# Performance work log

Hardware: AMD Instinct MI355X
Metric: run time of the kernel (lower is better)

The kernel has to match this reference:

```python
import jax, jax.numpy as jnp
import numpy as np

SR = 48000.0


def _lin_interp(x, n):
    # Matches torch F.interpolate(mode='linear', align_corners=False) on last axis.
    T = x.shape[-1]
    pos = (jnp.arange(n, dtype=jnp.float32) + 0.5) * (T / n) - 0.5
    pos = jnp.clip(pos, 0.0, T - 1)
    i0 = jnp.floor(pos).astype(jnp.int32)
    i1 = jnp.minimum(i0 + 1, T - 1)
    w = (pos - i0.astype(jnp.float32)).astype(x.dtype)
    return jnp.take(x, i0, axis=-1) * (1.0 - w) + jnp.take(x, i1, axis=-1) * w


def setup_inputs() -> dict:
    key = jax.random.key(0)
    k1, k2, k3 = jax.random.split(key, 3)
    B, T, N = 16, 250, 100
    harm_amps = jax.random.uniform(k1, (B, T, N), dtype=jnp.float32)
    # realistic fundamental frequencies: 80..480 Hz
    f0_hz = 80.0 + 400.0 * jax.random.uniform(k2, (B, T), dtype=jnp.float32)
    # small inharmonicity coefficients (piano-like): ~0..1e-4
    inh = 1e-4 * jax.random.uniform(k3, (B,), dtype=jnp.float32)
    return {"harm_amps": harm_amps, "f0_hz": f0_hz, "inh": inh, "n_samples": 48000}


def reference(harm_amps, f0_hz, inh, n_samples):
    B, T, N = harm_amps.shape
    # upsample amplitudes (B,N,n_samples) and f0 (B,n_samples)
    a = _lin_interp(jnp.transpose(harm_amps, (0, 2, 1)), n_samples)
    f0_up = _lin_interp(f0_hz, n_samples)
    k = jnp.arange(1, N + 1, dtype=jnp.float32)  # harmonic numbers 1..N
    stretch = jnp.sqrt(1.0 + inh[:, None] * k ** 2)  # (B,N)
    inst_freq = f0_up[:, None, :] * (k[None, :] * stretch)[:, :, None]  # (B,N,n)
    nyq_mask = (inst_freq < SR * 0.45).astype(a.dtype)
    phase = jnp.cumsum(2.0 * jnp.pi * inst_freq / SR, axis=-1)
    signal = jnp.sum(a * nyq_mask * jnp.sin(phase), axis=1, keepdims=True)  # (B,1,n)
    return signal / N
```

## Files before the change

kernel.cpp:

```cpp
#include <hip/hip_runtime.h>
#include <cmath>

#pragma clang fp contract(off)

#define SRF   48000.0f
#define NYQF  21600.0f
constexpr float  TWO_PI_F  = 6.283185307179586476925286766559f;
constexpr double INV_2PI_D = 0.15915494309189533576888376337251;
constexpr float  RC1 = (float)INV_2PI_D;
constexpr float  RC2 = (float)(INV_2PI_D - (double)RC1);
constexpr double INV_SR_D = 1.0 / 48000.0;
constexpr float  DD1 = (float)INV_SR_D;
constexpr float  DD2 = (float)(INV_SR_D - (double)DD1);

__device__ __forceinline__ float hsin_rev(float r) {
#if __has_builtin(__builtin_amdgcn_sinf)
    return __builtin_amdgcn_sinf(r);
#else
    return __sinf(r * TWO_PI_F);
#endif
}

__device__ __forceinline__ float div48000(float t) {
    float h = t * DD1;
    float r = __builtin_fmaf(t, DD1, -h);
    float s = __builtin_fmaf(t, DD2, r);
    return h + s;
}

__device__ __forceinline__ float sin_phase(float ph) {
    float h  = ph * RC1;
    float r  = __builtin_fmaf(ph, RC1, -h);
    float s  = __builtin_fmaf(ph, RC2, r);
    float nn = __builtin_rintf(h);
    float fr = (h - nn) + s;
    return hsin_rev(fr);
}

template <int IDX>
__device__ __forceinline__ float grp4_bcast(float v, int lb) {
#if __has_builtin(__builtin_amdgcn_ds_swizzle)
    constexpr int imm = (IDX << 5) | 0x1C;
    return __int_as_float(__builtin_amdgcn_ds_swizzle(__float_as_int(v), imm));
#else
    return __shfl(v, lb + IDX);
#endif
}

__device__ __forceinline__ float grp8_bcast0(float v, int lane) {
#if __has_builtin(__builtin_amdgcn_ds_swizzle)
    return __int_as_float(__builtin_amdgcn_ds_swizzle(__float_as_int(v), 0x0018));
#else
    return __shfl(v, lane & ~7);
#endif
}

__device__ __forceinline__ float pair_swap(float v) {
#if __has_builtin(__builtin_amdgcn_ds_swizzle)
    return __int_as_float(__builtin_amdgcn_ds_swizzle(__float_as_int(v), 0x041F));
#else
    return __shfl_xor(v, 1);
#endif
}

__device__ __forceinline__ float kcval(int k, float ib) {
    float kf = (float)(k + 1);
    float k2 = kf * kf;
    float m  = ib * k2;
    float s1 = 1.0f + m;
    float st = (float)sqrt((double)s1);
    return kf * st;
}

__global__ void __launch_bounds__(256) k_f0up(const float* __restrict__ f0,
        float* __restrict__ f0up, float* __restrict__ out,
        int T, int n, float pf) {
    int j = blockIdx.x * 256 + threadIdx.x;
    int b = blockIdx.y;
    if (j >= n) return;
    float pos = ((float)j + 0.5f);
    pos = pos * pf;
    pos = pos - 0.5f;
    pos = fmaxf(pos, 0.0f);
    pos = fminf(pos, (float)(T - 1));
    int   i0 = (int)pos;
    int   i1 = min(i0 + 1, T - 1);
    float w  = pos - (float)i0;
    float omw = 1.0f - w;
    const float* fb = f0 + b * T;
    f0up[(size_t)b * n + j] = fb[i0] * omw + fb[i1] * w;
    out[(size_t)b * n + j]  = 0.0f;
}

__global__ void __launch_bounds__(256) k_scan4(const float* __restrict__ f0up,
        const float* __restrict__ inh, float* __restrict__ scanS,
        int N, int n) {
    __shared__ float lv[3008];
    const int k   = blockIdx.x;
    const int b   = blockIdx.y;
    const int tid = threadIdx.x;
    const float kc = kcval(k, inh[b]);
    const float4* f4 = (const float4*)(f0up + (size_t)b * n);
    const int len4 = n >> 4;
    const int len5 = n >> 5;

    auto l2of = [&](float4 v) -> float {
        float a0 = div48000(TWO_PI_F * (kc * v.x));
        float a1 = div48000(TWO_PI_F * (kc * v.y));
        float a2 = div48000(TWO_PI_F * (kc * v.z));
        float a3 = div48000(TWO_PI_F * (kc * v.w));
        return (a0 + a1) + (a2 + a3);
    };
    auto l4of = [&](int j) -> float {
        float s01 = l2of(f4[4*j])     + l2of(f4[4*j + 1]);
        float s23 = l2of(f4[4*j + 2]) + l2of(f4[4*j + 3]);
        return s01 + s23;
    };
    for (int i = tid; i < len4; i += 256) {
        float v  = l4of(i);
        float vp = pair_swap(v);
        if ((i & 1) == 0) lv[i >> 1] = v + vp;
    }
    __syncthreads();

    int offp = 0, lenp = len5, P = 5;
    for (int l = 6; ; ++l) {
        int lenc = lenp >> 1;
        int offc = offp + lenp;
        for (int i = tid; i < lenc; i += 256)
            lv[offc + i] = lv[offp + 2*i] + lv[offp + 2*i + 1];
        __syncthreads();
        P = l;
        if (lenc == 1) break;
        offp = offc; lenp = lenc;
    }
    for (int l = P - 1; l >= 5; --l) {
        int lenl = n >> l;
        int offl = 0;
        for (int m = 5; m < l; ++m) offl += (n >> m);
        float*       arr = lv + offl;
        const float* hi  = lv + offl + lenl;
        int lenh = n >> (l + 1);
        for (int i = tid; i < lenh; i += 256) {
            float v = hi[i];
            int e = 2*i + 2;
            if (e < lenl) arr[e] = v + arr[e];
            arr[2*i + 1] = v;
        }
        __syncthreads();
    }
    float* sp = scanS + (size_t)(b * N + k) * (len5 + 1);
    if (tid == 0) sp[0] = 0.0f;
    for (int i = tid; i < len5; i += 256) sp[1 + i] = lv[i];
}

__global__ void __launch_bounds__(256) k_synth4(
        const float* __restrict__ harm, const float* __restrict__ f0up,
        const float* __restrict__ inh,  const float* __restrict__ scanS,
        float* __restrict__ out, int B, int T, int N, int n, float pf, int kpg) {
    const int tid  = threadIdx.x;
    const int b    = blockIdx.y;
    const int k0   = blockIdx.z * kpg;
    const int g    = blockIdx.x * 256 + tid;
    const int q    = g >> 2;
    const int c    = g & 3;
    const int NG   = n >> 4;
    const int NG5P = (n >> 5) + 1;
    const int kend = min(k0 + kpg, N);
    const int kact = kend - k0;
    const bool valid = q < NG;
    const bool oddq  = (q & 1) != 0;
    const int  si    = (q >> 1) + (q & 1);

    __shared__ float2 amps[8 * 32];
    __shared__ float  kcs[32];
    __shared__ float  xp[4][256];

    const float ib    = inh[b];
    const float tmaxf = (float)(T - 1);
    for (int i = tid; i < kact; i += 256) kcs[i] = kcval(k0 + i, ib);

    const int j0blk = blockIdx.x * 1024;
    int i0min;
    {
        float p = ((float)j0blk + 0.5f);
        p = p * pf; p = p - 0.5f;
        p = fmaxf(p, 0.0f); p = fminf(p, tmaxf);
        i0min = (int)p;
    }
    for (int idx = tid; idx < 8 * kact; idx += 256) {
        int r = idx / kact, kk = idx - r * kact;
        int r0 = min(i0min + r, T - 1);
        int r1 = min(i0min + r + 1, T - 1);
        float a0 = harm[((size_t)b * T + r0) * N + (k0 + kk)];
        float a1 = harm[((size_t)b * T + r1) * N + (k0 + kk)];
        amps[idx] = make_float2(a0, a1 - a0);
    }
    __syncthreads();

    float u0=0.f,u1=0.f,u2=0.f,u3=0.f;
    float w0=0.f,w1=0.f,w2=0.f,w3=0.f;
    int   a0o=0,a1o=0,a2o=0,a3o=0;
    float acc0=0.f, acc1=0.f, acc2=0.f, acc3=0.f;
    float um = __builtin_inff();
    if (valid) {
        const float4 v = *(const float4*)(f0up + (size_t)b * n + (size_t)q * 16 + c * 4);
        u0=v.x; u1=v.y; u2=v.z; u3=v.w;
        um = fminf(fminf(u0,u1), fminf(u2,u3));
        const int jb = q * 16 + c * 4;
        #pragma unroll
        for (int i = 0; i < 4; ++i) {
            float p = ((float)(jb + i) + 0.5f);
            p = p * pf; p = p - 0.5f;
            p = fmaxf(p, 0.0f); p = fminf(p, tmaxf);
            int i0 = (int)p;
            float wv = p - (float)i0;
            int aoo  = (i0 - i0min) * kact;
            if (i==0){w0=wv;a0o=aoo;}
            else if (i==1){w1=wv;a1o=aoo;}
            else if (i==2){w2=wv;a2o=aoo;}
            else {w3=wv;a3o=aoo;}
        }
    }
    #pragma unroll
    for (int off = 32; off > 0; off >>= 1)
        um = fminf(um, __shfl_xor(um, off));
    const float umin = um;
    const int lane = tid & 63;
    const int lb   = lane & ~3;

    if (valid) {
        const float* s4k = scanS + (size_t)(b * N + k0) * NG5P;
        float svc = s4k[si];

        for (int k = k0; k < kend; ++k) {
            const int   kk = k - k0;
            const float kc = kcs[kk];
            if (kc * umin >= NYQF) break;
            const float Sv = svc;
            if (k + 1 < kend) {
                const float* nx = s4k + NG5P;
                svc = nx[si];
                s4k = nx;
            }

            float x0 = div48000(TWO_PI_F * (kc * u0));
            float x1 = div48000(TWO_PI_F * (kc * u1));
            float x2 = div48000(TWO_PI_F * (kc * u2));
            float x3 = div48000(TWO_PI_F * (kc * u3));
            float L1p = x0 + x1, L1q = x2 + x3;
            float L2  = L1p + L1q;

            float s0 = grp4_bcast<0>(L2, lb);
            float s1 = grp4_bcast<1>(L2, lb);
            float s2 = grp4_bcast<2>(L2, lb);
            float s3 = grp4_bcast<3>(L2, lb);
            float t01 = s0 + s1;
            float s23 = s2 + s3;
            float L4v = t01 + s23;
            float G1e = Sv + L4v;
            float Gx  = grp8_bcast0(G1e, lane);
            float G0  = oddq ? Gx : Sv;
            float G1  = oddq ? Sv : G1e;

            float b1v = G0 + s0;
            float b2v = G0 + t01;
            float b3v = b2v + s2;
            float base = (c == 0) ? G0  : (c == 1) ? b1v : (c == 2) ? b2v : b3v;
            float bn   = (c == 0) ? b1v : (c == 1) ? b2v : (c == 2) ? b3v : G1;

            float ph0 = base + x0;
            float ph1 = base + L1p;
            float ph2 = ph1 + x2;
            float ph3 = bn;

            {   float t1 = kc * u0;
                if (t1 < NYQF) { float sv = sin_phase(ph0);
                    float2 a = amps[a0o + kk];
                    acc0 = __builtin_fmaf(__builtin_fmaf(w0, a.y, a.x), sv, acc0); } }
            {   float t1 = kc * u1;
                if (t1 < NYQF) { float sv = sin_phase(ph1);
                    float2 a = amps[a1o + kk];
                    acc1 = __builtin_fmaf(__builtin_fmaf(w1, a.y, a.x), sv, acc1); } }
            {   float t1 = kc * u2;
                if (t1 < NYQF) { float sv = sin_phase(ph2);
                    float2 a = amps[a2o + kk];
                    acc2 = __builtin_fmaf(__builtin_fmaf(w2, a.y, a.x), sv, acc2); } }
            {   float t1 = kc * u3;
                if (t1 < NYQF) { float sv = sin_phase(ph3);
                    float2 a = amps[a3o + kk];
                    acc3 = __builtin_fmaf(__builtin_fmaf(w3, a.y, a.x), sv, acc3); } }
        }
    }

    {
        const int wid  = tid >> 6;
        *(float4*)&xp[wid][4 * lane] = make_float4(acc0, acc1, acc2, acc3);
        const float Nf = (float)N;
        const int jb = blockIdx.x * 1024 + wid * 256;
        float* ob = out + (size_t)b * n + jb;
        #pragma unroll
        for (int i = 0; i < 4; ++i) {
            float v  = xp[wid][i * 64 + lane];
            int   jj = jb + i * 64 + lane;
            if (jj < n) atomicAdd(&ob[i * 64 + lane], v / Nf);
        }
    }
}

__global__ void __launch_bounds__(256) k_scan_synth(
        const float* __restrict__ harm, const float* __restrict__ f0up,
        const float* __restrict__ inh,  float* __restrict__ out,
        int B, int T, int N, int n, float pf) {
    extern __shared__ float lv[];
    const int k   = blockIdx.x;
    const int b   = blockIdx.y;
    const int tid = threadIdx.x;
    const float kc = kcval(k, inh[b]);
    const float* fb = f0up + (size_t)b * n;

    auto inc = [&](int j) -> float {
        float u    = fb[j];
        float inst = kc * u;
        float tt   = TWO_PI_F * inst;
        return tt / SRF;
    };

    const int len1 = n >> 1;
    {
        const float4* f4 = (const float4*)fb;
        for (int i = tid; i < (n >> 2); i += 256) {
            float4 u = f4[i];
            float a0 = (TWO_PI_F * (kc * u.x)) / SRF;
            float a1 = (TWO_PI_F * (kc * u.y)) / SRF;
            float a2 = (TWO_PI_F * (kc * u.z)) / SRF;
            float a3 = (TWO_PI_F * (kc * u.w)) / SRF;
            lv[i] = (a0 + a1) + (a2 + a3);
        }
    }
    __syncthreads();
    int offp = 0, lenp = n >> 2, P = 2;
    for (int l = 3; ; ++l) {
        int lenc = lenp >> 1;
        int offc = offp + lenp;
        for (int i = tid; i < lenc; i += 256)
            lv[offc + i] = lv[offp + 2*i] + lv[offp + 2*i + 1];
        __syncthreads();
        P = l;
        if (lenc == 1) break;
        offp = offc; lenp = lenc;
    }
    for (int l = P - 1; l >= 2; --l) {
        int lenl = n >> l;
        int offl = 0;
        for (int m = 2; m < l; ++m) offl += (n >> m);
        float*       arr = lv + offl;
        const float* hi  = lv + offl + lenl;
        int lenh = n >> (l + 1);
        for (int i = tid; i < lenh; i += 256) {
            float v = hi[i];
            int e = 2*i + 2;
            if (e < lenl) arr[e] = v + arr[e];
            arr[2*i + 1] = v;
        }
        __syncthreads();
    }
    const float* scan2 = lv;

    const float  tmaxf = (float)(T - 1);
    const float  invN  = 1.0f / (float)N;
    const float* hb    = harm + (size_t)b * T * N + k;
    float*       ob    = out + (size_t)b * n;

    auto emit = [&](int j, float ph) {
        float u    = fb[j];
        float inst = kc * u;
        if (!(inst < NYQF)) return;
        double pr = (double)ph * INV_2PI_D;
        double fr = pr - rint(pr);
        float  sv = hsin_rev((float)fr);
        float pos = ((float)j + 0.5f);
        pos = pos * pf; pos = pos - 0.5f;
        pos = fmaxf(pos, 0.0f); pos = fminf(pos, tmaxf);
        int   i0 = (int)pos;
        int   i1 = min(i0 + 1, T - 1);
        float w  = pos - (float)i0;
        float a  = hb[(size_t)i0 * N] * (1.0f - w) + hb[(size_t)i1 * N] * w;
        atomicAdd(&ob[j], (a * sv) * invN);
    };

    if (tid == 0) emit(0, inc(0));
    for (int tt = tid; tt < len1; tt += 256) {
        float s1;
        if (tt == 0)      s1 = inc(0) + inc(1);
        else if (tt & 1)  s1 = scan2[(tt - 1) >> 1];
        else              s1 = scan2[(tt >> 1) - 1] + (inc(2*tt) + inc(2*tt + 1));
        emit(2*tt + 1, s1);
        int je = 2*tt + 2;
        if (je < n) emit(je, s1 + inc(je));
    }
}

extern "C" void kernel_launch(void* const* d_in, const int* in_sizes, int n_in,
                              void* d_out, int out_size, void* d_ws, size_t ws_size,
                              hipStream_t stream) {
    const int B = in_sizes[2];
    const int T = in_sizes[1] / B;
    const int N = in_sizes[0] / (B * T);
    const int n = out_size / B;
    const float pf = (float)((double)T / (double)n);

    const float* harm = (const float*)d_in[0];
    const float* f0   = (const float*)d_in[1];
    const float* inh  = (const float*)d_in[2];
    float* out  = (float*)d_out;
    float* f0up = (float*)d_ws;

    const int KZ  = 4;
    const int kpg = (N + KZ - 1) / KZ;
    const int NG  = n / 16;
    const int NG5 = n / 32;
    const size_t needFast = (size_t)B * n * 4 + (size_t)B * N * (NG5 + 1) * 4;
    const bool fast = (ws_size >= needFast) && (n % 32 == 0) && (kpg <= 32);

    k_f0up<<<dim3((n + 255) / 256, B), 256, 0, stream>>>(f0, f0up, out, T, n, pf);

    if (fast) {
        float* scanS = (float*)((char*)d_ws + (size_t)B * n * 4);
        k_scan4<<<dim3(N, B), 256, 0, stream>>>(f0up, inh, scanS, N, n);
        const int tiles = (NG * 4 + 255) / 256;
        k_synth4<<<dim3(tiles, B, KZ), 256, 0, stream>>>(
            harm, f0up, inh, scanS, out, B, T, N, n, pf, kpg);
    } else {
        const size_t lds_bytes = (size_t)(n / 2) * sizeof(float);
        k_scan_synth<<<dim3(N, B), 256, lds_bytes, stream>>>(
            harm, f0up, inh, out, B, T, N, n, pf);
    }
}
```

Measured before the change: 135.9 us.

## Fuse f0 upsample, scan and synthesis into one cooperative persistent kernel

Replaces the three separate launches (f0 upsample, per-harmonic scan, synthesis) with a single cooperative kernel that runs a persistent grid and uses grid-wide syncs between the phases. The aim is to remove launch overhead and inter-kernel gaps. The grid is sized from occupancy times CU count, and the old three-kernel path remains as a fallback if the cooperative launch fails. The cost is two grid.sync barriers, and the work loops are now limited to the resident block count rather than the original grid shapes.

```diff
diff --git a/kernel.cpp b/kernel.cpp
--- a/kernel.cpp
+++ b/kernel.cpp
@@ -1,5 +1,8 @@
 #include <hip/hip_runtime.h>
+#include <hip/hip_cooperative_groups.h>
 #include <cmath>
+
+namespace cg = cooperative_groups;
 
 #pragma clang fp contract(off)
 
@@ -70,6 +73,254 @@
     float s1 = 1.0f + m;
     float st = (float)sqrt((double)s1);
     return kf * st;
+}
+
+__global__ void __launch_bounds__(256) k_fused(
+        const float* __restrict__ harm, const float* __restrict__ f0,
+        const float* __restrict__ inh,  float* __restrict__ f0up,
+        float* __restrict__ scanS,      float* __restrict__ out,
+        int B, int T, int N, int n, float pf, int kpg, int tiles, int KZ) {
+    cg::grid_group gridg = cg::this_grid();
+    __shared__ float lv[3008];
+    const int tid = threadIdx.x;
+    const int G   = gridDim.x;
+    const float tmaxf = (float)(T - 1);
+    const int len4 = n >> 4;
+    const int len5 = n >> 5;
+    const int NG   = n >> 4;
+    const int NG5P = (n >> 5) + 1;
+
+    {
+        const long total = (long)B * n;
+        for (long idx = (long)blockIdx.x * 256 + tid; idx < total;
+             idx += (long)G * 256) {
+            int b = (int)(idx / n);
+            int j = (int)(idx - (long)b * n);
+            float pos = ((float)j + 0.5f);
+            pos = pos * pf;
+            pos = pos - 0.5f;
+            pos = fmaxf(pos, 0.0f);
+            pos = fminf(pos, tmaxf);
+            int   i0 = (int)pos;
+            int   i1 = min(i0 + 1, T - 1);
+            float w  = pos - (float)i0;
+            float omw = 1.0f - w;
+            const float* fb = f0 + b * T;
+            f0up[idx] = fb[i0] * omw + fb[i1] * w;
+            out[idx]  = 0.0f;
+        }
+    }
+    gridg.sync();
+
+    for (int vb = blockIdx.x; vb < N * B; vb += G) {
+        const int k = vb % N;
+        const int b = vb / N;
+        const float kc = kcval(k, inh[b]);
+        const float4* f4 = (const float4*)(f0up + (size_t)b * n);
+
+        auto l2of = [&](float4 v) -> float {
+            float a0 = div48000(TWO_PI_F * (kc * v.x));
+            float a1 = div48000(TWO_PI_F * (kc * v.y));
+            float a2 = div48000(TWO_PI_F * (kc * v.z));
+            float a3 = div48000(TWO_PI_F * (kc * v.w));
+            return (a0 + a1) + (a2 + a3);
+        };
+        auto l4of = [&](int j) -> float {
+            float s01 = l2of(f4[4*j])     + l2of(f4[4*j + 1]);
+            float s23 = l2of(f4[4*j + 2]) + l2of(f4[4*j + 3]);
+            return s01 + s23;
+        };
+        for (int i = tid; i < len4; i += 256) {
+            float v  = l4of(i);
+            float vp = pair_swap(v);
+            if ((i & 1) == 0) lv[i >> 1] = v + vp;
+        }
+        __syncthreads();
+
+        int offp = 0, lenp = len5, P = 5;
+        for (int l = 6; ; ++l) {
+            int lenc = lenp >> 1;
+            int offc = offp + lenp;
+            for (int i = tid; i < lenc; i += 256)
+                lv[offc + i] = lv[offp + 2*i] + lv[offp + 2*i + 1];
+            __syncthreads();
+            P = l;
+            if (lenc == 1) break;
+            offp = offc; lenp = lenc;
+        }
+        for (int l = P - 1; l >= 5; --l) {
+            int lenl = n >> l;
+            int offl = 0;
+            for (int m = 5; m < l; ++m) offl += (n >> m);
+            float*       arr = lv + offl;
+            const float* hi  = lv + offl + lenl;
+            int lenh = n >> (l + 1);
+            for (int i = tid; i < lenh; i += 256) {
+                float v = hi[i];
+                int e = 2*i + 2;
+                if (e < lenl) arr[e] = v + arr[e];
+                arr[2*i + 1] = v;
+            }
+            __syncthreads();
+        }
+        float* sp = scanS + (size_t)(b * N + k) * (len5 + 1);
+        if (tid == 0) sp[0] = 0.0f;
+        for (int i = tid; i < len5; i += 256) sp[1 + i] = lv[i];
+        __syncthreads();
+    }
+    gridg.sync();
+
+    float2* amps = (float2*)lv;
+    float*  kcs  = lv + 512;
+    float*  xp   = lv + 544;
+    const int totC = tiles * B * KZ;
+    const int lane = tid & 63;
+    const int lb   = lane & ~3;
+
+    for (int vs = blockIdx.x; vs < totC; vs += G) {
+        const int tile = vs % tiles;
+        const int rb   = vs / tiles;
+        const int b    = rb % B;
+        const int z    = rb / B;
+        const int k0   = z * kpg;
+        const int g2   = tile * 256 + tid;
+        const int q    = g2 >> 2;
+        const int c    = g2 & 3;
+        const int kend = min(k0 + kpg, N);
+        const int kact = kend - k0;
+        const bool valid = q < NG;
+        const bool oddq  = (q & 1) != 0;
+        const int  si    = (q >> 1) + (q & 1);
+
+        const float ib = inh[b];
+        for (int i = tid; i < kact; i += 256) kcs[i] = kcval(k0 + i, ib);
+
+        const int j0blk = tile * 1024;
+        int i0min;
+        {
+            float p = ((float)j0blk + 0.5f);
+            p = p * pf; p = p - 0.5f;
+            p = fmaxf(p, 0.0f); p = fminf(p, tmaxf);
+            i0min = (int)p;
+        }
+        for (int idx = tid; idx < 8 * kact; idx += 256) {
+            int r = idx / kact, kk = idx - r * kact;
+            int r0 = min(i0min + r, T - 1);
+            int r1 = min(i0min + r + 1, T - 1);
+            float a0 = harm[((size_t)b * T + r0) * N + (k0 + kk)];
+            float a1 = harm[((size_t)b * T + r1) * N + (k0 + kk)];
+            amps[idx] = make_float2(a0, a1 - a0);
+        }
+        __syncthreads();
+
+        float u0=0.f,u1=0.f,u2=0.f,u3=0.f;
+        float w0=0.f,w1=0.f,w2=0.f,w3=0.f;
+        int   a0o=0,a1o=0,a2o=0,a3o=0;
+        float acc0=0.f, acc1=0.f, acc2=0.f, acc3=0.f;
+        float um = __builtin_inff();
+        if (valid) {
+            const float4 v = *(const float4*)(f0up + (size_t)b * n + (size_t)q * 16 + c * 4);
+            u0=v.x; u1=v.y; u2=v.z; u3=v.w;
+            um = fminf(fminf(u0,u1), fminf(u2,u3));
+            const int jb = q * 16 + c * 4;
+            #pragma unroll
+            for (int i = 0; i < 4; ++i) {
+                float p = ((float)(jb + i) + 0.5f);
+                p = p * pf; p = p - 0.5f;
+                p = fmaxf(p, 0.0f); p = fminf(p, tmaxf);
+                int i0 = (int)p;
+                float wv = p - (float)i0;
+                int aoo  = (i0 - i0min) * kact;
+                if (i==0){w0=wv;a0o=aoo;}
+                else if (i==1){w1=wv;a1o=aoo;}
+                else if (i==2){w2=wv;a2o=aoo;}
+                else {w3=wv;a3o=aoo;}
+            }
+        }
+        #pragma unroll
+        for (int off = 32; off > 0; off >>= 1)
+            um = fminf(um, __shfl_xor(um, off));
+        const float umin = um;
+
+        if (valid) {
+            const float* s4k = scanS + (size_t)(b * N + k0) * NG5P;
+            float svc = s4k[si];
+
+            for (int k = k0; k < kend; ++k) {
+                const int   kk = k - k0;
+                const float kc = kcs[kk];
+                if (kc * umin >= NYQF) break;
+                const float Sv = svc;
+                if (k + 1 < kend) {
+                    const float* nx = s4k + NG5P;
+                    svc = nx[si];
+                    s4k = nx;
+                }
+
+                float x0 = div48000(TWO_PI_F * (kc * u0));
+                float x1 = div48000(TWO_PI_F * (kc * u1));
+                float x2 = div48000(TWO_PI_F * (kc * u2));
+                float x3 = div48000(TWO_PI_F * (kc * u3));
+                float L1p = x0 + x1, L1q = x2 + x3;
+                float L2  = L1p + L1q;
+
+                float s0 = grp4_bcast<0>(L2, lb);
+                float s1 = grp4_bcast<1>(L2, lb);
+                float s2 = grp4_bcast<2>(L2, lb);
+                float s3 = grp4_bcast<3>(L2, lb);
+                float t01 = s0 + s1;
+                float s23 = s2 + s3;
+                float L4v = t01 + s23;
+                float G1e = Sv + L4v;
+                float Gx  = grp8_bcast0(G1e, lane);
+                float G0  = oddq ? Gx : Sv;
+                float G1  = oddq ? Sv : G1e;
+
+                float b1v = G0 + s0;
+                float b2v = G0 + t01;
+                float b3v = b2v + s2;
+                float base = (c == 0) ? G0  : (c == 1) ? b1v : (c == 2) ? b2v : b3v;
+                float bn   = (c == 0) ? b1v : (c == 1) ? b2v : (c == 2) ? b3v : G1;
+
+                float ph0 = base + x0;
+                float ph1 = base + L1p;
+                float ph2 = ph1 + x2;
+                float ph3 = bn;
+
+                {   float t1 = kc * u0;
+                    if (t1 < NYQF) { float sv = sin_phase(ph0);
+                        float2 a = amps[a0o + kk];
+                        acc0 = __builtin_fmaf(__builtin_fmaf(w0, a.y, a.x), sv, acc0); } }
+                {   float t1 = kc * u1;
+                    if (t1 < NYQF) { float sv = sin_phase(ph1);
+                        float2 a = amps[a1o + kk];
+                        acc1 = __builtin_fmaf(__builtin_fmaf(w1, a.y, a.x), sv, acc1); } }
+                {   float t1 = kc * u2;
+                    if (t1 < NYQF) { float sv = sin_phase(ph2);
+                        float2 a = amps[a2o + kk];
+                        acc2 = __builtin_fmaf(__builtin_fmaf(w2, a.y, a.x), sv, acc2); } }
+                {   float t1 = kc * u3;
+                    if (t1 < NYQF) { float sv = sin_phase(ph3);
+                        float2 a = amps[a3o + kk];
+                        acc3 = __builtin_fmaf(__builtin_fmaf(w3, a.y, a.x), sv, acc3); } }
+            }
+        }
+
+        {
+            const int wid = tid >> 6;
+            *(float4*)&xp[wid * 256 + 4 * lane] = make_float4(acc0, acc1, acc2, acc3);
+            const float Nf = (float)N;
+            const int jb = tile * 1024 + wid * 256;
+            float* ob = out + (size_t)b * n + jb;
+            #pragma unroll
+            for (int i = 0; i < 4; ++i) {
+                float v  = xp[wid * 256 + i * 64 + lane];
+                int   jj = jb + i * 64 + lane;
+                if (jj < n) atomicAdd(&ob[i * 64 + lane], v / Nf);
+            }
+        }
+        __syncthreads();
+    }
 }
 
 __global__ void __launch_bounds__(256) k_f0up(const float* __restrict__ f0,
@@ -420,18 +671,55 @@
     const int kpg = (N + KZ - 1) / KZ;
     const int NG  = n / 16;
     const int NG5 = n / 32;
+    const int tiles = (NG * 4 + 255) / 256;
     const size_t needFast = (size_t)B * n * 4 + (size_t)B * N * (NG5 + 1) * 4;
     const bool fast = (ws_size >= needFast) && (n % 32 == 0) && (kpg <= 32);
 
-    k_f0up<<<dim3((n + 255) / 256, B), 256, 0, stream>>>(f0, f0up, out, T, n, pf);
-
     if (fast) {
         float* scanS = (float*)((char*)d_ws + (size_t)B * n * 4);
-        k_scan4<<<dim3(N, B), 256, 0, stream>>>(f0up, inh, scanS, N, n);
-        const int tiles = (NG * 4 + 255) / 256;
-        k_synth4<<<dim3(tiles, B, KZ), 256, 0, stream>>>(
-            harm, f0up, inh, scanS, out, B, T, N, n, pf, kpg);
+
+        static int s_G = -2;
+        if (s_G == -2) {
+            int dev = 0;
+            (void)hipGetDevice(&dev);
+            int coop = 0;
+            (void)hipDeviceGetAttribute(&coop, hipDeviceAttributeCooperativeLaunch, dev);
+            int numCU = 0;
+            (void)hipDeviceGetAttribute(&numCU, hipDeviceAttributeMultiprocessorCount, dev);
+            int bpc = 0;
+            (void)hipOccupancyMaxActiveBlocksPerMultiprocessor(&bpc, k_fused, 256, 0);
+            s_G = (coop && bpc > 0 && numCU > 0) ? bpc * numCU : 0;
+        }
+
+        bool done = false;
+        if (s_G > 0) {
+            const float* a_harm = harm; const float* a_f0 = f0;
+            const float* a_inh = inh;   float* a_f0up = f0up;
+            float* a_scanS = scanS;     float* a_out = out;
+            int a_B = B, a_T = T, a_N = N, a_n = n;
+            float a_pf = pf; int a_kpg = kpg, a_tiles = tiles, a_KZ = KZ;
+            void* args[] = { (void*)&a_harm, (void*)&a_f0, (void*)&a_inh,
+                             (void*)&a_f0up, (void*)&a_scanS, (void*)&a_out,
+                             (void*)&a_B, (void*)&a_T, (void*)&a_N, (void*)&a_n,
+                             (void*)&a_pf, (void*)&a_kpg, (void*)&a_tiles,
+                             (void*)&a_KZ };
+            hipError_t e = hipLaunchCooperativeKernel(k_fused, dim3(s_G),
+                                                      dim3(256), args, 0, stream);
+            if (e == hipSuccess) {
+                done = true;
+            } else {
+                (void)hipGetLastError();
+                s_G = 0;
+            }
+        }
+        if (!done) {
+            k_f0up<<<dim3((n + 255) / 256, B), 256, 0, stream>>>(f0, f0up, out, T, n, pf);
+            k_scan4<<<dim3(N, B), 256, 0, stream>>>(f0up, inh, scanS, N, n);
+            k_synth4<<<dim3(tiles, B, KZ), 256, 0, stream>>>(
+                harm, f0up, inh, scanS, out, B, T, N, n, pf, kpg);
+        }
     } else {
+        k_f0up<<<dim3((n + 255) / 256, B), 256, 0, stream>>>(f0, f0up, out, T, n, pf);
         const size_t lds_bytes = (size_t)(n / 2) * sizeof(float);
         k_scan_synth<<<dim3(N, B), 256, lds_bytes, stream>>>(
             harm, f0up, inh, out, B, T, N, n, pf);
```

Result: slower. 346.1 us (+154.7%).
